# Kernel tuning notes

Hardware: AMD Instinct MI355X
Metric: run time of the kernel (lower is better)

## Reference

```python
import jax, jax.numpy as jnp
import numpy as np

N = 100000      # nodes
E = 800000      # edges
IN1 = 128       # gcn input feature dim
IN2 = 64        # lstm input feature dim
H = 128         # hidden_channels
B = 32          # lstm batch
T = 200         # lstm seq len
OUT = 1         # out_channels
TARGET = jnp.array([0, 1000, 2000, 3000, 4000, 5000, 6000, 7000])  # numgcnE=8


def setup_inputs() -> dict:
    key = jax.random.key(0)
    ks = jax.random.split(key, 20)
    s = 0.05
    inp = {
        "data0": jax.random.normal(ks[0], (B, T, IN2), jnp.float32),
        "data1": jax.random.normal(ks[1], (N, IN1), jnp.float32),
        "edge_index": jax.random.randint(ks[2], (2, E), 0, N, dtype=jnp.int64),
        # GCNConv layers (weight stored [in, out])
        "W1": jax.random.normal(ks[3], (IN1, H), jnp.float32) * s,
        "b1": jnp.zeros((H,), jnp.float32),
        "W2": jax.random.normal(ks[4], (H, H), jnp.float32) * s,
        "b2": jnp.zeros((H,), jnp.float32),
        # LSTM1 (gate order i,f,g,o as in torch)
        "Wih1": jax.random.normal(ks[5], (4 * H, IN2), jnp.float32) * s,
        "Whh1": jax.random.normal(ks[6], (4 * H, H), jnp.float32) * s,
        "bih1": jnp.zeros((4 * H,), jnp.float32),
        "bhh1": jnp.zeros((4 * H,), jnp.float32),
        # LSTM2
        "Wih2": jax.random.normal(ks[7], (4 * H, H), jnp.float32) * s,
        "Whh2": jax.random.normal(ks[8], (4 * H, H), jnp.float32) * s,
        "bih2": jnp.zeros((4 * H,), jnp.float32),
        "bhh2": jnp.zeros((4 * H,), jnp.float32),
        # MLP head: (numgcnE+1)*H -> (numgcnE+1)*H/2 -> OUT
        "m1_w": jax.random.normal(ks[9], (9 * H, 9 * H // 2), jnp.float32) * s,
        "m1_b": jnp.zeros((9 * H // 2,), jnp.float32),
        "m2_w": jax.random.normal(ks[10], (9 * H // 2, OUT), jnp.float32) * s,
        "m2_b": jnp.zeros((OUT,), jnp.float32),
    }
    return inp


def gcn_conv(x, W, b, src, dst, n):
    # PyG GCNConv: self-loops + symmetric normalization, then scatter-add.
    xw = x @ W                                                     # [N, H]
    ones = jnp.ones(src.shape[0], xw.dtype)
    deg = jax.ops.segment_sum(ones, dst, num_segments=n) + 1.0     # +1 self-loop
    dinv = jax.lax.rsqrt(deg)                                      # [N]
    norm = dinv[src] * dinv[dst]                                   # [E]
    agg = jax.ops.segment_sum(xw[src] * norm[:, None], dst, num_segments=n)
    agg = agg + xw * (dinv * dinv)[:, None]                        # self-loop msgs
    return agg + b


def lstm_final(x_tbi, Wih, Whh, bih, bhh):
    # x_tbi: [T, Bsz, in]; returns final hidden state h_T [Bsz, H]
    Bsz = x_tbi.shape[1]
    Hh = Whh.shape[1]
    bias = bih + bhh

    def step(carry, xt):
        h, c = carry
        g = xt @ Wih.T + h @ Whh.T + bias                          # [Bsz, 4H]
        i, f, gg, o = jnp.split(g, 4, axis=-1)
        c = jax.nn.sigmoid(f) * c + jax.nn.sigmoid(i) * jnp.tanh(gg)
        h = jax.nn.sigmoid(o) * jnp.tanh(c)
        return (h, c), None

    init = (jnp.zeros((Bsz, Hh), x_tbi.dtype), jnp.zeros((Bsz, Hh), x_tbi.dtype))
    (h, c), _ = jax.lax.scan(step, init, x_tbi)
    return h


def reference(data0, data1, edge_index, W1, b1, W2, b2,
              Wih1, Whh1, bih1, bhh1, Wih2, Whh2, bih2, bhh2,
              m1_w, m1_b, m2_w, m2_b):
    src, dst = edge_index[0], edge_index[1]
    n = data1.shape[0]
    # two GCN layers with ReLU
    h = jax.nn.relu(gcn_conv(data1, W1, b1, src, dst, n))
    h = jax.nn.relu(gcn_conv(h, W2, b2, src, dst, n))
    g = h[TARGET].reshape(-1)                                      # [numgcnE*H]
    # lstm1 over [B, T, IN2] (batch_first) -> final h_n [B, H]
    h1 = lstm_final(jnp.swapaxes(data0, 0, 1), Wih1, Whh1, bih1, bhh1)
    # lstm2 consumes h_n[None] as [batch=1, seq=B, H] -> final h [1, H]
    h2 = lstm_final(h1[:, None, :], Wih2, Whh2, bih2, bhh2)[0]     # [H]
    d = jnp.concatenate([g, h2])                                   # [(numgcnE+1)*H]
    return (d @ m1_w + m1_b) @ m2_w + m2_b                         # [OUT]
```

## Files before the change

### kernel.cpp

```cpp
#include <hip/hip_runtime.h>
#include <hip/hip_bf16.h>
#include <cstring>

using bf16 = __hip_bfloat16;
typedef _Float16 h2v __attribute__((ext_vector_type(2)));
typedef _Float16 h8v __attribute__((ext_vector_type(8)));

#if __has_builtin(__builtin_amdgcn_fdot2)
__device__ __forceinline__ float FDOT2(h2v a, h2v b, float c) {
    return __builtin_amdgcn_fdot2(a, b, c, false);
}
#else
__device__ __forceinline__ float FDOT2(h2v a, h2v b, float c) {
    return c + (float)a.x * (float)b.x + (float)a.y * (float)b.y;
}
#endif

__device__ __forceinline__ float sigm_f(float x) {
    return __builtin_amdgcn_rcpf(1.f + __expf(-x));
}
__device__ __forceinline__ float tanh_f(float x) {
    return 1.f - 2.f * __builtin_amdgcn_rcpf(1.f + __expf(2.f * x));
}

constexpr int NH    = 128;
constexpr int G4    = 512;
constexpr int TSEQ  = 200;
constexpr int BBATCH= 32;
constexpr int NTGT  = 8;

constexpr int LCAP1 = 1024;
constexpr int S1CAP = LCAP1 + NTGT;
constexpr int LCAP2 = 8192;
constexpr int S2CAP = LCAP2 + S1CAP;

constexpr size_t algn(size_t x) { return (x + 255) & ~size_t(255); }
constexpr size_t OFF_GX1  = 0;
constexpr size_t OFF_GX2  = algn(OFF_GX1  + 6400ull * G4 * 4);
constexpr size_t OFF_DEG  = algn(OFF_GX2  + 32ull * G4 * 4);
constexpr size_t OFF_DINV = algn(OFF_DEG  + 100000ull * 4);
constexpr size_t OFF_SL1  = algn(OFF_DINV + 100000ull * 4);
constexpr size_t OFF_SL2  = algn(OFF_SL1  + 100000ull * 4);
constexpr size_t OFF_CNT  = algn(OFF_SL2  + 100000ull * 4);
constexpr size_t OFF_L1   = algn(OFF_CNT  + 64);
constexpr size_t OFF_S1   = algn(OFF_L1   + (size_t)LCAP1 * 8);
constexpr size_t OFF_L2   = algn(OFF_S1   + (size_t)S1CAP * 4);
constexpr size_t OFF_S2   = algn(OFF_L2   + (size_t)LCAP2 * 8);
constexpr size_t OFF_XW1  = algn(OFF_S2   + (size_t)S2CAP * 4);
constexpr size_t OFF_H1   = algn(OFF_XW1  + (size_t)S2CAP * NH * 4);
constexpr size_t OFF_XW2  = algn(OFF_H1   + (size_t)S1CAP * NH * 4);
constexpr size_t OFF_DVEC = algn(OFF_XW2  + (size_t)S1CAP * NH * 4);
constexpr size_t OFF_H1F  = algn(OFF_DVEC + 1152ull * 4);
constexpr size_t OFF_CACC = algn(OFF_H1F  + 32ull * NH * 4);
constexpr size_t WS_NEEDED = OFF_CACC + 576ull * 4;

__device__ __forceinline__ int edge_at(const int* ei, int E, int is64, int row, int e) {
    return is64 ? ei[(((size_t)row * E) + e) * 2] : ei[((size_t)row * E) + e];
}

__device__ __forceinline__ float dinv_of(const int* deg, int v) {
    return rsqrtf((float)deg[v] + 1.0f);
}

__global__ void k_canary(unsigned int* out, unsigned int bits) {
    if (threadIdx.x == 0) out[0] = bits;
}


__global__ void k_init(const int* ei, int* deg, int* slot1, int* slot2, int* cnt,
                       float* colacc, int n) {
    int i = blockIdx.x * 256 + threadIdx.x;
    if (i < 14) cnt[i] = 0;
    if (i == 15) cnt[15] = (ei[1] == 0 && ei[3] == 0 && ei[5] == 0 && ei[7] == 0) ? 1 : 0;
    if (i < 576) colacc[i] = 0.f;
    for (; i < n; i += gridDim.x * 256) { deg[i] = 0; slot1[i] = -1; slot2[i] = -1; }
}

__global__ void k_deg_l1(const int* ei, int E, int* deg, int2* l1, int* cnt) {
    int is64 = cnt[15];
    for (int e = blockIdx.x * 256 + threadIdx.x; e < E; e += gridDim.x * 256) {
        int d = edge_at(ei, E, is64, 1, e);
        if ((unsigned)d < 100000u) atomicAdd(&deg[d], 1);
        if (d <= 7000 && d >= 0 && d % 1000 == 0) {
            int s = edge_at(ei, E, is64, 0, e);
            int idx = atomicAdd(&cnt[0], 1);
            if (idx < LCAP1) l1[idx] = make_int2(s, d);
        }
    }
}

__global__ void k_s1(const int2* l1, int* cnt, int* slot1, int* s1list,
                     int* slot2, int* s2list) {
    __shared__ int ns1;
    if (threadIdx.x == 0) ns1 = 0;
    __syncthreads();
    int m = min(cnt[0], LCAP1);
    for (int i = threadIdx.x; i < NTGT + m; i += blockDim.x) {
        int v = (i < NTGT) ? i * 1000 : l1[i - NTGT].x;
        if ((unsigned)v >= 100000u) continue;
        int old = atomicCAS(&slot1[v], -1, -2);
        if (old == -1) {
            int idx = atomicAdd(&ns1, 1);
            if (idx < S1CAP) { s1list[idx] = v; atomicExch(&slot1[v], idx); }
        }
    }
    __syncthreads();
    int n1 = min(ns1, S1CAP);
    if (threadIdx.x == 0) cnt[1] = n1;
    for (int i = threadIdx.x; i < n1; i += blockDim.x) {
        int v = s1list[i];
        int old = atomicCAS(&slot2[v], -1, -2);
        if (old == -1) {
            int idx = atomicAdd(&cnt[2], 1);
            if (idx < S2CAP) { s2list[idx] = v; atomicExch(&slot2[v], idx); }
        }
    }
}

__global__ void k_l2(const int* ei, int E, const int* slot1,
                     int2* l2, int* cnt, int* slot2, int* s2list) {
    int is64 = cnt[15];
    for (int e = blockIdx.x * 256 + threadIdx.x; e < E; e += gridDim.x * 256) {
        int d = edge_at(ei, E, is64, 1, e);
        if ((unsigned)d >= 100000u) continue;
        if (slot1[d] >= 0) {
            int s = edge_at(ei, E, is64, 0, e);
            if ((unsigned)s >= 100000u) continue;
            int idx = atomicAdd(&cnt[3], 1);
            if (idx < LCAP2) l2[idx] = make_int2(s, d);
            int old = atomicCAS(&slot2[s], -1, -2);
            if (old == -1) {
                int j = atomicAdd(&cnt[2], 1);
                if (j < S2CAP) { s2list[j] = s; atomicExch(&slot2[s], j); }
            }
        }
    }
}


__global__ void k_xw1(const float* x, const float* W, const int* s2list, const int* cnt, float* xw1) {
    int i = blockIdx.x;
    if (i >= min(cnt[2], S2CAP)) return;
    int node = s2list[i];
    __shared__ float xs[NH];
    int c = threadIdx.x;
    xs[c] = x[(size_t)node * NH + c];
    __syncthreads();
    float acc = 0.f;
    #pragma unroll 8
    for (int k = 0; k < NH; k++) acc += xs[k] * W[(size_t)k * NH + c];
    xw1[(size_t)i * NH + c] = acc;
}

__global__ void k_h1init(const float* xw1, const int* s1list, const int* cnt,
                         const int* slot2, const int* deg, float* h1) {
    int i = blockIdx.x;
    if (i >= min(cnt[1], S1CAP)) return;
    int node = s1list[i];
    int s2 = slot2[node];
    if (s2 < 0 || s2 >= S2CAP) s2 = 0;
    float v = dinv_of(deg, node);
    h1[i * NH + threadIdx.x] = xw1[(size_t)s2 * NH + threadIdx.x] * v * v;
}

__global__ void k_h1scat(const float* xw1, const int2* l2, const int* cnt,
                         const int* slot1, const int* slot2, const int* deg, float* h1) {
    int e = blockIdx.x;
    if (e >= min(cnt[3], LCAP2)) return;
    int2 sd = l2[e];
    int t1 = slot1[sd.y], s2 = slot2[sd.x];
    if (t1 < 0 || t1 >= S1CAP || s2 < 0 || s2 >= S2CAP) return;
    float w = dinv_of(deg, sd.x) * dinv_of(deg, sd.y);
    atomicAdd(&h1[t1 * NH + threadIdx.x],
              xw1[(size_t)s2 * NH + threadIdx.x] * w);
}

__global__ void k_xw2(const float* h1, const float* W, const float* b1, const int* cnt, float* xw2) {
    int i = blockIdx.x;
    if (i >= min(cnt[1], S1CAP)) return;
    __shared__ float xs[NH];
    int c = threadIdx.x;
    xs[c] = fmaxf(h1[i * NH + c] + b1[c], 0.f);
    __syncthreads();
    float acc = 0.f;
    #pragma unroll 8
    for (int k = 0; k < NH; k++) acc += xs[k] * W[(size_t)k * NH + c];
    xw2[(size_t)i * NH + c] = acc;
}

__global__ void k_gout(const float* xw2, const int2* l1, const int* cnt,
                       const int* slot1, const int* deg, const float* b2, float* dvec) {
    int t = blockIdx.x;
    int tgt = t * 1000;
    int c = threadIdx.x;
    float vt = dinv_of(deg, tgt);
    int st = slot1[tgt]; if (st < 0 || st >= S1CAP) st = 0;
    float acc = xw2[(size_t)st * NH + c] * vt * vt;
    int m = min(cnt[0], LCAP1);
    for (int e = 0; e < m; e++) {
        int2 sd = l1[e];
        if (sd.y == tgt) {
            int ss = slot1[sd.x];
            if (ss >= 0 && ss < S1CAP)
                acc += xw2[(size_t)ss * NH + c] * dinv_of(deg, sd.x) * vt;
        }
    }
    acc += b2[c];
    dvec[t * NH + c] = fmaxf(acc, 0.f);
}


__global__ __launch_bounds__(256) void k_gx1(const float* data0, const float* Wih,
                                             const float* bih, const float* bhh, float* gx) {
    constexpr int LDP = 68;
    __shared__ float As[64 * LDP];
    __shared__ float Bs[64 * LDP];
    int tid = threadIdx.x;
    int rb = blockIdx.x >> 3;
    int gb = blockIdx.x & 7;
    int r0 = rb * 64, g0 = gb * 64;
    for (int i = tid; i < 64 * 64; i += 256) {
        int rr = i >> 6, k = i & 63;
        int r = r0 + rr, b = r & 31, t = r >> 5;
        As[rr * LDP + k] = data0[((size_t)b * TSEQ + t) * 64 + k];
        Bs[rr * LDP + k] = Wih[(size_t)(g0 + rr) * 64 + k];
    }
    __syncthreads();
    int tr = (tid & 15) * 4;
    int tg = (tid >> 4) * 4;
    float acc[4][4] = {};
    #pragma unroll
    for (int k4 = 0; k4 < 16; k4++) {
        float4 a0 = *(const float4*)&As[(tr + 0) * LDP + k4 * 4];
        float4 a1 = *(const float4*)&As[(tr + 1) * LDP + k4 * 4];
        float4 a2 = *(const float4*)&As[(tr + 2) * LDP + k4 * 4];
        float4 a3 = *(const float4*)&As[(tr + 3) * LDP + k4 * 4];
        float4 b0 = *(const float4*)&Bs[(tg + 0) * LDP + k4 * 4];
        float4 b1 = *(const float4*)&Bs[(tg + 1) * LDP + k4 * 4];
        float4 b2 = *(const float4*)&Bs[(tg + 2) * LDP + k4 * 4];
        float4 b3 = *(const float4*)&Bs[(tg + 3) * LDP + k4 * 4];
        const float4 av[4] = {a0, a1, a2, a3};
        const float4 bv[4] = {b0, b1, b2, b3};
        #pragma unroll
        for (int i = 0; i < 4; i++)
            #pragma unroll
            for (int j = 0; j < 4; j++)
                acc[i][j] += av[i].x * bv[j].x + av[i].y * bv[j].y
                           + av[i].z * bv[j].z + av[i].w * bv[j].w;
    }
    float bias[4];
    #pragma unroll
    for (int j = 0; j < 4; j++) bias[j] = bih[g0 + tg + j] + bhh[g0 + tg + j];
    #pragma unroll
    for (int i = 0; i < 4; i++) {
        size_t row = (size_t)(r0 + tr + i) * G4 + g0 + tg;
        #pragma unroll
        for (int j = 0; j < 4; j++) gx[row + j] = acc[i][j] + bias[j];
    }
}

__global__ void k_gx2(const float* h1f, const float* Wih,
                      const float* bih, const float* bhh, float* gx) {
    int t = blockIdx.x;
    __shared__ float xs[NH];
    int tid = threadIdx.x;
    int g0 = tid, g1 = tid + 256;
    if (tid < NH) xs[tid] = h1f[t * NH + tid];
    __syncthreads();
    float a0 = bih[g0] + bhh[g0];
    float a1 = bih[g1] + bhh[g1];
    #pragma unroll 4
    for (int k = 0; k < NH; k++) {
        a0 += Wih[(size_t)g0 * NH + k] * xs[k];
        a1 += Wih[(size_t)g1 * NH + k] * xs[k];
    }
    gx[(size_t)t * G4 + g0] = a0;
    gx[(size_t)t * G4 + g1] = a1;
}

template<int T, int NB>
__global__ __launch_bounds__(256, 1) void k_lstm(const float* gx, const float* Whh, float* hfinal) {
    int b = blockIdx.x;
    int tid = threadIdx.x;
    int w = tid >> 6, l = tid & 63;
    int j = w * 32 + (l & 31);
    int role = l >> 5;
    int r0 = role ? (j + NH) : j;
    int r1 = role ? (j + 3 * NH) : (j + 2 * NH);
    __shared__ __align__(16) _Float16 hbuf[2][NH];
    h2v w0[NH / 2], w1[NH / 2];
    #pragma unroll
    for (int k = 0; k < NH; k += 4) {
        float4 a = *(const float4*)&Whh[(size_t)r0 * NH + k];
        w0[k / 2]     = h2v{(_Float16)a.x, (_Float16)a.y};
        w0[k / 2 + 1] = h2v{(_Float16)a.z, (_Float16)a.w};
        float4 c4 = *(const float4*)&Whh[(size_t)r1 * NH + k];
        w1[k / 2]     = h2v{(_Float16)c4.x, (_Float16)c4.y};
        w1[k / 2 + 1] = h2v{(_Float16)c4.z, (_Float16)c4.w};
    }
    if (tid < NH) { hbuf[0][tid] = (_Float16)0.f; hbuf[1][tid] = (_Float16)0.f; }
    float c = 0.f, hout = 0.f;
    float nx0 = gx[((size_t)0 * NB + b) * G4 + r0];
    float nx1 = gx[((size_t)0 * NB + b) * G4 + r1];
    __syncthreads();
    for (int t = 0; t < T; t++) {
        const h8v* hv8 = (const h8v*)hbuf[t & 1];
        float a0 = nx0, a1 = nx1;
        int tn = (t + 1 < T) ? (t + 1) : t;
        nx0 = gx[((size_t)tn * NB + b) * G4 + r0];
        nx1 = gx[((size_t)tn * NB + b) * G4 + r1];
        float p0 = 0.f, q0 = 0.f, p1 = 0.f, q1 = 0.f;
        #pragma unroll
        for (int m = 0; m < NH / 8; m++) {
            h8v h8 = hv8[m];
            h2v ha = __builtin_shufflevector(h8, h8, 0, 1);
            h2v hb = __builtin_shufflevector(h8, h8, 2, 3);
            h2v hc = __builtin_shufflevector(h8, h8, 4, 5);
            h2v hd = __builtin_shufflevector(h8, h8, 6, 7);
            p0 = FDOT2(w0[4 * m],     ha, p0);
            q0 = FDOT2(w0[4 * m + 1], hb, q0);
            p0 = FDOT2(w0[4 * m + 2], hc, p0);
            q0 = FDOT2(w0[4 * m + 3], hd, q0);
            p1 = FDOT2(w1[4 * m],     ha, p1);
            q1 = FDOT2(w1[4 * m + 1], hb, q1);
            p1 = FDOT2(w1[4 * m + 2], hc, p1);
            q1 = FDOT2(w1[4 * m + 3], hd, q1);
        }
        float ga = a0 + p0 + q0;
        float gb = a1 + p1 + q1;
        float s  = sigm_f(ga);
        float tg = role ? sigm_f(gb) : tanh_f(gb);
        float u  = s * tg;
        float fv = __shfl_xor(s,  32);
        float ov = __shfl_xor(tg, 32);
        if (role == 0) {
            c = fv * c + u;
            hout = ov * tanh_f(c);
            hbuf[(t + 1) & 1][j] = (_Float16)hout;
        }
        __syncthreads();
    }
    if (role == 0) hfinal[(size_t)b * NH + j] = hout;
}

__global__ __launch_bounds__(64) void k_head1(const float* dvec, const float* m1w, float* colacc) {
    int rg = blockIdx.x & 7;
    int cg = blockIdx.x >> 3;
    int col = cg * 64 + threadIdx.x;
    int r0 = rg * 144;
    float acc = 0.f;
    #pragma unroll 4
    for (int i = r0; i < r0 + 144; i++)
        acc += dvec[i] * m1w[(size_t)i * 576 + col];
    atomicAdd(&colacc[col], acc);
}

__global__ __launch_bounds__(256) void k_head2(const float* colacc, const float* m1b,
                                               const float* m2w, const float* m2b,
                                               unsigned int* out) {
    __shared__ float wr[4];
    int j = threadIdx.x;
    float sum = 0.f;
    for (int col = j; col < 576; col += 256)
        sum += (colacc[col] + m1b[col]) * m2w[col];
    #pragma unroll
    for (int off = 32; off > 0; off >>= 1) sum += __shfl_down(sum, off, 64);
    if ((j & 63) == 0) wr[j >> 6] = sum;
    __syncthreads();
    if (j == 0) {
        float s = wr[0] + wr[1] + wr[2] + wr[3] + m2b[0];
        bf16 hb = __float2bfloat16(s);
        unsigned short u;
        memcpy(&u, &hb, 2);
        out[0] = ((unsigned int)u << 16) | u;
    }
}


extern "C" void kernel_launch(void* const* d_in, const int* in_sizes, int n_in,
                              void* d_out, int out_size, void* d_ws, size_t ws_size,
                              hipStream_t stream) {
    const float* data0 = (const float*)d_in[0];
    const float* data1 = (const float*)d_in[1];
    const int*   ei    = (const int*)d_in[2];
    const float* W1    = (const float*)d_in[3];
    const float* b1    = (const float*)d_in[4];
    const float* W2    = (const float*)d_in[5];
    const float* b2    = (const float*)d_in[6];
    const float* Wih1  = (const float*)d_in[7];
    const float* Whh1  = (const float*)d_in[8];
    const float* bih1  = (const float*)d_in[9];
    const float* bhh1  = (const float*)d_in[10];
    const float* Wih2  = (const float*)d_in[11];
    const float* Whh2  = (const float*)d_in[12];
    const float* bih2  = (const float*)d_in[13];
    const float* bhh2  = (const float*)d_in[14];
    const float* m1w   = (const float*)d_in[15];
    const float* m1b   = (const float*)d_in[16];
    const float* m2w   = (const float*)d_in[17];
    const float* m2b   = (const float*)d_in[18];

    const int n = in_sizes[1] / NH;
    const int E = in_sizes[2] / 2;

    char* ws = (char*)d_ws;
    float* gx1   = (float*)(ws + OFF_GX1);
    float* gx2   = (float*)(ws + OFF_GX2);
    int*   deg   = (int*)  (ws + OFF_DEG);
    int*   slot1 = (int*)  (ws + OFF_SL1);
    int*   slot2 = (int*)  (ws + OFF_SL2);
    int*   cnt   = (int*)  (ws + OFF_CNT);
    int2*  l1    = (int2*) (ws + OFF_L1);
    int*   s1l   = (int*)  (ws + OFF_S1);
    int2*  l2    = (int2*) (ws + OFF_L2);
    int*   s2l   = (int*)  (ws + OFF_S2);
    float* xw1   = (float*)(ws + OFF_XW1);
    float* h1    = (float*)(ws + OFF_H1);
    float* xw2   = (float*)(ws + OFF_XW2);
    float* dvec  = (float*)(ws + OFF_DVEC);
    float* h1f   = (float*)(ws + OFF_H1F);
    float* cacc  = (float*)(ws + OFF_CACC);

    float v = 1.0f + (ws_size < WS_NEEDED ? 1.0f : 0.0f) + (n_in != 19 ? 2.0f : 0.0f);
    unsigned int fb; memcpy(&fb, &v, 4);
    unsigned int hi = fb >> 16;
    unsigned int canary_bits = (hi << 16) | hi;
    k_canary <<<1, 64, 0, stream>>>((unsigned int*)d_out, canary_bits);

    int nb = (n + 255) / 256;
    int eb = (E + 255) / 256;

    k_init   <<<nb, 256, 0, stream>>>(ei, deg, slot1, slot2, cnt, cacc, n);
    k_deg_l1 <<<eb, 256, 0, stream>>>(ei, E, deg, l1, cnt);
    k_s1     <<<1, 256, 0, stream>>>(l1, cnt, slot1, s1l, slot2, s2l);
    k_l2     <<<eb, 256, 0, stream>>>(ei, E, slot1, l2, cnt, slot2, s2l);
    k_xw1    <<<S2CAP, NH, 0, stream>>>(data1, W1, s2l, cnt, xw1);
    k_h1init <<<S1CAP, NH, 0, stream>>>(xw1, s1l, cnt, slot2, deg, h1);
    k_h1scat <<<LCAP2, NH, 0, stream>>>(xw1, l2, cnt, slot1, slot2, deg, h1);
    k_xw2    <<<S1CAP, NH, 0, stream>>>(h1, W2, b1, cnt, xw2);
    k_gout   <<<NTGT, NH, 0, stream>>>(xw2, l1, cnt, slot1, deg, b2, dvec);
    k_gx1    <<<800, 256, 0, stream>>>(data0, Wih1, bih1, bhh1, gx1);
    k_lstm<TSEQ, BBATCH><<<BBATCH, 256, 0, stream>>>(gx1, Whh1, h1f);
    k_gx2    <<<BBATCH, 256, 0, stream>>>(h1f, Wih2, bih2, bhh2, gx2);
    k_lstm<BBATCH, 1>  <<<1, 256, 0, stream>>>(gx2, Whh2, dvec + 1024);
    k_head1  <<<72, 64, 0, stream>>>(dvec, m1w, cacc);
    k_head2  <<<1, 256, 0, stream>>>(cacc, m1b, m2w, m2b, (unsigned int*)d_out);
    (void)out_size;
}
```

Measured before the change: 403.3 us.

## Fuse GCN pipeline into one cooperative kernel with grid syncs

Result: slower. 802.5 us (+99.0%).

```diff
diff --git a/kernel.cpp b/kernel.cpp
--- a/kernel.cpp
+++ b/kernel.cpp
@@ -1,6 +1,9 @@
 #include <hip/hip_runtime.h>
+#include <hip/hip_cooperative_groups.h>
 #include <hip/hip_bf16.h>
 #include <cstring>
+
+namespace cg = cooperative_groups;
 
 using bf16 = __hip_bfloat16;
 typedef _Float16 h2v __attribute__((ext_vector_type(2)));
@@ -21,6 +24,18 @@
 }
 __device__ __forceinline__ float tanh_f(float x) {
     return 1.f - 2.f * __builtin_amdgcn_rcpf(1.f + __expf(2.f * x));
+}
+
+__device__ __forceinline__ float xor32_get(float x) {
+#if __has_builtin(__builtin_amdgcn_permlane32_swap)
+    typedef unsigned uv2 __attribute__((ext_vector_type(2)));
+    union { float f; unsigned u; } cv; cv.f = x;
+    uv2 r = __builtin_amdgcn_permlane32_swap(cv.u, cv.u, false, false);
+    union { unsigned u; float f; } rv; rv.u = r[1];
+    return rv.f;
+#else
+    return __shfl_xor(x, 32);
+#endif
 }
 
 constexpr int NH    = 128;
@@ -33,6 +48,8 @@
 constexpr int S1CAP = LCAP1 + NTGT;
 constexpr int LCAP2 = 8192;
 constexpr int S2CAP = LCAP2 + S1CAP;
+
+constexpr int GCN_BLOCKS = 512;
 
 constexpr size_t algn(size_t x) { return (x + 255) & ~size_t(255); }
 constexpr size_t OFF_GX1  = 0;
@@ -62,151 +79,155 @@
     return rsqrtf((float)deg[v] + 1.0f);
 }
 
-__global__ void k_canary(unsigned int* out, unsigned int bits) {
-    if (threadIdx.x == 0) out[0] = bits;
-}
-
-
-__global__ void k_init(const int* ei, int* deg, int* slot1, int* slot2, int* cnt,
-                       float* colacc, int n) {
-    int i = blockIdx.x * 256 + threadIdx.x;
-    if (i < 14) cnt[i] = 0;
-    if (i == 15) cnt[15] = (ei[1] == 0 && ei[3] == 0 && ei[5] == 0 && ei[7] == 0) ? 1 : 0;
-    if (i < 576) colacc[i] = 0.f;
-    for (; i < n; i += gridDim.x * 256) { deg[i] = 0; slot1[i] = -1; slot2[i] = -1; }
-}
-
-__global__ void k_deg_l1(const int* ei, int E, int* deg, int2* l1, int* cnt) {
-    int is64 = cnt[15];
-    for (int e = blockIdx.x * 256 + threadIdx.x; e < E; e += gridDim.x * 256) {
-        int d = edge_at(ei, E, is64, 1, e);
-        if ((unsigned)d < 100000u) atomicAdd(&deg[d], 1);
+
+struct GcnArgs {
+    const int* ei; int E; int n;
+    int* deg; int* slot1; int* slot2; int* cnt;
+    int2* l1; int* s1l; int2* l2; int* s2l;
+    const float* data1; const float* W1; const float* b1;
+    const float* W2; const float* b2;
+    float* xw1; float* h1; float* xw2; float* dvec; float* colacc;
+    unsigned int* out; unsigned int canary;
+};
+
+__global__ __launch_bounds__(256) void k_gcn(GcnArgs a) {
+    cg::grid_group grid = cg::this_grid();
+    const int tid = threadIdx.x;
+    const int gid = blockIdx.x * 256 + tid;
+    const int gstride = gridDim.x * 256;
+    const int half = tid >> 7;
+    const int c    = tid & 127;
+
+    if (gid == 0) a.out[0] = a.canary;
+    if (gid < 14) a.cnt[gid] = 0;
+    if (gid == 15) a.cnt[15] = (a.ei[1] == 0 && a.ei[3] == 0 && a.ei[5] == 0 && a.ei[7] == 0) ? 1 : 0;
+    if (gid < 576) a.colacc[gid] = 0.f;
+    for (int i = gid; i < a.n; i += gstride) { a.deg[i] = 0; a.slot1[i] = -1; a.slot2[i] = -1; }
+    for (int i = gid; i < S1CAP * NH; i += gstride) a.h1[i] = 0.f;
+    grid.sync();
+
+    const int is64 = a.cnt[15];
+    for (int e = gid; e < a.E; e += gstride) {
+        int d = edge_at(a.ei, a.E, is64, 1, e);
+        if ((unsigned)d < 100000u) atomicAdd(&a.deg[d], 1);
         if (d <= 7000 && d >= 0 && d % 1000 == 0) {
-            int s = edge_at(ei, E, is64, 0, e);
-            int idx = atomicAdd(&cnt[0], 1);
-            if (idx < LCAP1) l1[idx] = make_int2(s, d);
-        }
-    }
-}
-
-__global__ void k_s1(const int2* l1, int* cnt, int* slot1, int* s1list,
-                     int* slot2, int* s2list) {
+            int s = edge_at(a.ei, a.E, is64, 0, e);
+            int idx = atomicAdd(&a.cnt[0], 1);
+            if (idx < LCAP1) a.l1[idx] = make_int2(s, d);
+        }
+    }
+    grid.sync();
+
     __shared__ int ns1;
-    if (threadIdx.x == 0) ns1 = 0;
-    __syncthreads();
-    int m = min(cnt[0], LCAP1);
-    for (int i = threadIdx.x; i < NTGT + m; i += blockDim.x) {
-        int v = (i < NTGT) ? i * 1000 : l1[i - NTGT].x;
-        if ((unsigned)v >= 100000u) continue;
-        int old = atomicCAS(&slot1[v], -1, -2);
-        if (old == -1) {
-            int idx = atomicAdd(&ns1, 1);
-            if (idx < S1CAP) { s1list[idx] = v; atomicExch(&slot1[v], idx); }
-        }
-    }
-    __syncthreads();
-    int n1 = min(ns1, S1CAP);
-    if (threadIdx.x == 0) cnt[1] = n1;
-    for (int i = threadIdx.x; i < n1; i += blockDim.x) {
-        int v = s1list[i];
-        int old = atomicCAS(&slot2[v], -1, -2);
-        if (old == -1) {
-            int idx = atomicAdd(&cnt[2], 1);
-            if (idx < S2CAP) { s2list[idx] = v; atomicExch(&slot2[v], idx); }
-        }
-    }
-}
-
-__global__ void k_l2(const int* ei, int E, const int* slot1,
-                     int2* l2, int* cnt, int* slot2, int* s2list) {
-    int is64 = cnt[15];
-    for (int e = blockIdx.x * 256 + threadIdx.x; e < E; e += gridDim.x * 256) {
-        int d = edge_at(ei, E, is64, 1, e);
+    if (blockIdx.x == 0) {
+        if (tid == 0) ns1 = 0;
+        __syncthreads();
+        int m = min(a.cnt[0], LCAP1);
+        for (int i = tid; i < NTGT + m; i += 256) {
+            int v = (i < NTGT) ? i * 1000 : a.l1[i - NTGT].x;
+            if ((unsigned)v >= 100000u) continue;
+            int old = atomicCAS(&a.slot1[v], -1, -2);
+            if (old == -1) {
+                int idx = atomicAdd(&ns1, 1);
+                if (idx < S1CAP) { a.s1l[idx] = v; atomicExch(&a.slot1[v], idx); }
+            }
+        }
+        __syncthreads();
+        int n1 = min(ns1, S1CAP);
+        if (tid == 0) a.cnt[1] = n1;
+        for (int i = tid; i < n1; i += 256) {
+            int v = a.s1l[i];
+            int old = atomicCAS(&a.slot2[v], -1, -2);
+            if (old == -1) {
+                int idx = atomicAdd(&a.cnt[2], 1);
+                if (idx < S2CAP) { a.s2l[idx] = v; atomicExch(&a.slot2[v], idx); }
+            }
+        }
+    }
+    grid.sync();
+
+    for (int e = gid; e < a.E; e += gstride) {
+        int d = edge_at(a.ei, a.E, is64, 1, e);
         if ((unsigned)d >= 100000u) continue;
-        if (slot1[d] >= 0) {
-            int s = edge_at(ei, E, is64, 0, e);
+        if (a.slot1[d] >= 0) {
+            int s = edge_at(a.ei, a.E, is64, 0, e);
             if ((unsigned)s >= 100000u) continue;
-            int idx = atomicAdd(&cnt[3], 1);
-            if (idx < LCAP2) l2[idx] = make_int2(s, d);
-            int old = atomicCAS(&slot2[s], -1, -2);
+            int idx = atomicAdd(&a.cnt[3], 1);
+            if (idx < LCAP2) a.l2[idx] = make_int2(s, d);
+            int old = atomicCAS(&a.slot2[s], -1, -2);
             if (old == -1) {
-                int j = atomicAdd(&cnt[2], 1);
-                if (j < S2CAP) { s2list[j] = s; atomicExch(&slot2[s], j); }
+                int j = atomicAdd(&a.cnt[2], 1);
+                if (j < S2CAP) { a.s2l[j] = s; atomicExch(&a.slot2[s], j); }
             }
         }
     }
-}
-
-
-__global__ void k_xw1(const float* x, const float* W, const int* s2list, const int* cnt, float* xw1) {
-    int i = blockIdx.x;
-    if (i >= min(cnt[2], S2CAP)) return;
-    int node = s2list[i];
-    __shared__ float xs[NH];
-    int c = threadIdx.x;
-    xs[c] = x[(size_t)node * NH + c];
-    __syncthreads();
-    float acc = 0.f;
-    #pragma unroll 8
-    for (int k = 0; k < NH; k++) acc += xs[k] * W[(size_t)k * NH + c];
-    xw1[(size_t)i * NH + c] = acc;
-}
-
-__global__ void k_h1init(const float* xw1, const int* s1list, const int* cnt,
-                         const int* slot2, const int* deg, float* h1) {
-    int i = blockIdx.x;
-    if (i >= min(cnt[1], S1CAP)) return;
-    int node = s1list[i];
-    int s2 = slot2[node];
-    if (s2 < 0 || s2 >= S2CAP) s2 = 0;
-    float v = dinv_of(deg, node);
-    h1[i * NH + threadIdx.x] = xw1[(size_t)s2 * NH + threadIdx.x] * v * v;
-}
-
-__global__ void k_h1scat(const float* xw1, const int2* l2, const int* cnt,
-                         const int* slot1, const int* slot2, const int* deg, float* h1) {
-    int e = blockIdx.x;
-    if (e >= min(cnt[3], LCAP2)) return;
-    int2 sd = l2[e];
-    int t1 = slot1[sd.y], s2 = slot2[sd.x];
-    if (t1 < 0 || t1 >= S1CAP || s2 < 0 || s2 >= S2CAP) return;
-    float w = dinv_of(deg, sd.x) * dinv_of(deg, sd.y);
-    atomicAdd(&h1[t1 * NH + threadIdx.x],
-              xw1[(size_t)s2 * NH + threadIdx.x] * w);
-}
-
-__global__ void k_xw2(const float* h1, const float* W, const float* b1, const int* cnt, float* xw2) {
-    int i = blockIdx.x;
-    if (i >= min(cnt[1], S1CAP)) return;
-    __shared__ float xs[NH];
-    int c = threadIdx.x;
-    xs[c] = fmaxf(h1[i * NH + c] + b1[c], 0.f);
-    __syncthreads();
-    float acc = 0.f;
-    #pragma unroll 8
-    for (int k = 0; k < NH; k++) acc += xs[k] * W[(size_t)k * NH + c];
-    xw2[(size_t)i * NH + c] = acc;
-}
-
-__global__ void k_gout(const float* xw2, const int2* l1, const int* cnt,
-                       const int* slot1, const int* deg, const float* b2, float* dvec) {
-    int t = blockIdx.x;
-    int tgt = t * 1000;
-    int c = threadIdx.x;
-    float vt = dinv_of(deg, tgt);
-    int st = slot1[tgt]; if (st < 0 || st >= S1CAP) st = 0;
-    float acc = xw2[(size_t)st * NH + c] * vt * vt;
-    int m = min(cnt[0], LCAP1);
-    for (int e = 0; e < m; e++) {
-        int2 sd = l1[e];
-        if (sd.y == tgt) {
-            int ss = slot1[sd.x];
-            if (ss >= 0 && ss < S1CAP)
-                acc += xw2[(size_t)ss * NH + c] * dinv_of(deg, sd.x) * vt;
-        }
-    }
-    acc += b2[c];
-    dvec[t * NH + c] = fmaxf(acc, 0.f);
+    grid.sync();
+
+    {
+        int m2 = min(a.cnt[2], S2CAP);
+        for (int i = blockIdx.x * 2 + half; i < m2; i += gridDim.x * 2) {
+            int node = a.s2l[i];
+            const float* xr = &a.data1[(size_t)node * NH];
+            float acc = 0.f;
+            #pragma unroll 8
+            for (int k = 0; k < NH; k++) acc += xr[k] * a.W1[(size_t)k * NH + c];
+            a.xw1[(size_t)i * NH + c] = acc;
+        }
+    }
+    grid.sync();
+
+    {
+        int m3 = min(a.cnt[3], LCAP2);
+        for (int e = blockIdx.x * 2 + half; e < m3; e += gridDim.x * 2) {
+            int2 sd = a.l2[e];
+            int t1 = a.slot1[sd.y], s2 = a.slot2[sd.x];
+            if (t1 < 0 || t1 >= S1CAP || s2 < 0 || s2 >= S2CAP) continue;
+            float wgt = dinv_of(a.deg, sd.x) * dinv_of(a.deg, sd.y);
+            atomicAdd(&a.h1[(size_t)t1 * NH + c], a.xw1[(size_t)s2 * NH + c] * wgt);
+        }
+    }
+    grid.sync();
+
+    {
+        int m1 = min(a.cnt[1], S1CAP);
+        for (int i = blockIdx.x * 2 + half; i < m1; i += gridDim.x * 2) {
+            int node = a.s1l[i];
+            int s2i = a.slot2[node];
+            if (s2i < 0 || s2i >= S2CAP) s2i = 0;
+            float v = dinv_of(a.deg, node);
+            float vv = v * v;
+            const float* hr = &a.h1[(size_t)i * NH];
+            const float* br = &a.xw1[(size_t)s2i * NH];
+            float acc = 0.f;
+            #pragma unroll 8
+            for (int k = 0; k < NH; k++) {
+                float xk = fmaxf(hr[k] + br[k] * vv + a.b1[k], 0.f);
+                acc += xk * a.W2[(size_t)k * NH + c];
+            }
+            a.xw2[(size_t)i * NH + c] = acc;
+        }
+    }
+    grid.sync();
+
+    {
+        int m = min(a.cnt[0], LCAP1);
+        for (int t = blockIdx.x * 2 + half; t < NTGT; t += gridDim.x * 2) {
+            int tgt = t * 1000;
+            float vt = dinv_of(a.deg, tgt);
+            int st = a.slot1[tgt]; if (st < 0 || st >= S1CAP) st = 0;
+            float acc = a.xw2[(size_t)st * NH + c] * vt * vt;
+            for (int e = 0; e < m; e++) {
+                int2 sd = a.l1[e];
+                if (sd.y == tgt) {
+                    int ss = a.slot1[sd.x];
+                    if (ss >= 0 && ss < S1CAP)
+                        acc += a.xw2[(size_t)ss * NH + c] * dinv_of(a.deg, sd.x) * vt;
+                }
+            }
+            acc += a.b2[c];
+            a.dvec[t * NH + c] = fmaxf(acc, 0.f);
+        }
+    }
 }
 
 
@@ -331,8 +352,8 @@
         float s  = sigm_f(ga);
         float tg = role ? sigm_f(gb) : tanh_f(gb);
         float u  = s * tg;
-        float fv = __shfl_xor(s,  32);
-        float ov = __shfl_xor(tg, 32);
+        float fv = xor32_get(s);
+        float ov = xor32_get(tg);
         if (role == 0) {
             c = fv * c + u;
             hout = ov * tanh_f(c);
@@ -425,20 +446,18 @@
     unsigned int fb; memcpy(&fb, &v, 4);
     unsigned int hi = fb >> 16;
     unsigned int canary_bits = (hi << 16) | hi;
-    k_canary <<<1, 64, 0, stream>>>((unsigned int*)d_out, canary_bits);
-
-    int nb = (n + 255) / 256;
-    int eb = (E + 255) / 256;
-
-    k_init   <<<nb, 256, 0, stream>>>(ei, deg, slot1, slot2, cnt, cacc, n);
-    k_deg_l1 <<<eb, 256, 0, stream>>>(ei, E, deg, l1, cnt);
-    k_s1     <<<1, 256, 0, stream>>>(l1, cnt, slot1, s1l, slot2, s2l);
-    k_l2     <<<eb, 256, 0, stream>>>(ei, E, slot1, l2, cnt, slot2, s2l);
-    k_xw1    <<<S2CAP, NH, 0, stream>>>(data1, W1, s2l, cnt, xw1);
-    k_h1init <<<S1CAP, NH, 0, stream>>>(xw1, s1l, cnt, slot2, deg, h1);
-    k_h1scat <<<LCAP2, NH, 0, stream>>>(xw1, l2, cnt, slot1, slot2, deg, h1);
-    k_xw2    <<<S1CAP, NH, 0, stream>>>(h1, W2, b1, cnt, xw2);
-    k_gout   <<<NTGT, NH, 0, stream>>>(xw2, l1, cnt, slot1, deg, b2, dvec);
+
+    GcnArgs ga;
+    ga.ei = ei; ga.E = E; ga.n = n;
+    ga.deg = deg; ga.slot1 = slot1; ga.slot2 = slot2; ga.cnt = cnt;
+    ga.l1 = l1; ga.s1l = s1l; ga.l2 = l2; ga.s2l = s2l;
+    ga.data1 = data1; ga.W1 = W1; ga.b1 = b1; ga.W2 = W2; ga.b2 = b2;
+    ga.xw1 = xw1; ga.h1 = h1; ga.xw2 = xw2; ga.dvec = dvec; ga.colacc = cacc;
+    ga.out = (unsigned int*)d_out; ga.canary = canary_bits;
+    void* gcn_params[1] = { &ga };
+    (void)hipLaunchCooperativeKernel((const void*)k_gcn, dim3(GCN_BLOCKS), dim3(256),
+                                     gcn_params, 0, stream);
+
     k_gx1    <<<800, 256, 0, stream>>>(data0, Wih1, bih1, bhh1, gx1);
     k_lstm<TSEQ, BBATCH><<<BBATCH, 256, 0, stream>>>(gx1, Whh1, h1f);
     k_gx2    <<<BBATCH, 256, 0, stream>>>(h1f, Wih2, bih2, bhh2, gx2);
```

## Fuse LSTM2 with head, precompute collapsed MLP weights, merge small kernels

Applied to the files above, without the earlier changes.

Result: slower. 480.4 us (+19.1%).

```diff
diff --git a/kernel.cpp b/kernel.cpp
--- a/kernel.cpp
+++ b/kernel.cpp
@@ -21,6 +21,18 @@
 }
 __device__ __forceinline__ float tanh_f(float x) {
     return 1.f - 2.f * __builtin_amdgcn_rcpf(1.f + __expf(2.f * x));
+}
+
+__device__ __forceinline__ float xor32_get(float x) {
+#if __has_builtin(__builtin_amdgcn_permlane32_swap)
+    typedef unsigned uv2 __attribute__((ext_vector_type(2)));
+    union { float f; unsigned u; } cv; cv.f = x;
+    uv2 r = __builtin_amdgcn_permlane32_swap(cv.u, cv.u, false, false);
+    union { unsigned u; float f; } rv; rv.u = r[1];
+    return rv.f;
+#else
+    return __shfl_xor(x, 32);
+#endif
 }
 
 constexpr int NH    = 128;
@@ -62,18 +74,15 @@
     return rsqrtf((float)deg[v] + 1.0f);
 }
 
-__global__ void k_canary(unsigned int* out, unsigned int bits) {
-    if (threadIdx.x == 0) out[0] = bits;
-}
-
-
 __global__ void k_init(const int* ei, int* deg, int* slot1, int* slot2, int* cnt,
-                       float* colacc, int n) {
-    int i = blockIdx.x * 256 + threadIdx.x;
-    if (i < 14) cnt[i] = 0;
-    if (i == 15) cnt[15] = (ei[1] == 0 && ei[3] == 0 && ei[5] == 0 && ei[7] == 0) ? 1 : 0;
-    if (i < 576) colacc[i] = 0.f;
-    for (; i < n; i += gridDim.x * 256) { deg[i] = 0; slot1[i] = -1; slot2[i] = -1; }
+                       float* h1, int n, unsigned int* out, unsigned int canary) {
+    int i0 = blockIdx.x * 256 + threadIdx.x;
+    int gstride = gridDim.x * 256;
+    if (i0 < 14) cnt[i0] = 0;
+    if (i0 == 15) cnt[15] = (ei[1] == 0 && ei[3] == 0 && ei[5] == 0 && ei[7] == 0) ? 1 : 0;
+    if (i0 == 16) out[0] = canary;
+    for (int i = i0; i < S1CAP * NH; i += gstride) h1[i] = 0.f;
+    for (int i = i0; i < n; i += gstride) { deg[i] = 0; slot1[i] = -1; slot2[i] = -1; }
 }
 
 __global__ void k_deg_l1(const int* ei, int E, int* deg, int2* l1, int* cnt) {
@@ -152,17 +161,6 @@
     xw1[(size_t)i * NH + c] = acc;
 }
 
-__global__ void k_h1init(const float* xw1, const int* s1list, const int* cnt,
-                         const int* slot2, const int* deg, float* h1) {
-    int i = blockIdx.x;
-    if (i >= min(cnt[1], S1CAP)) return;
-    int node = s1list[i];
-    int s2 = slot2[node];
-    if (s2 < 0 || s2 >= S2CAP) s2 = 0;
-    float v = dinv_of(deg, node);
-    h1[i * NH + threadIdx.x] = xw1[(size_t)s2 * NH + threadIdx.x] * v * v;
-}
-
 __global__ void k_h1scat(const float* xw1, const int2* l2, const int* cnt,
                          const int* slot1, const int* slot2, const int* deg, float* h1) {
     int e = blockIdx.x;
@@ -175,12 +173,18 @@
               xw1[(size_t)s2 * NH + threadIdx.x] * w);
 }
 
-__global__ void k_xw2(const float* h1, const float* W, const float* b1, const int* cnt, float* xw2) {
+__global__ void k_xw2(const float* h1, const float* xw1, const float* W, const float* b1,
+                      const int* cnt, const int* s1list, const int* slot2, const int* deg,
+                      float* xw2) {
     int i = blockIdx.x;
     if (i >= min(cnt[1], S1CAP)) return;
     __shared__ float xs[NH];
     int c = threadIdx.x;
-    xs[c] = fmaxf(h1[i * NH + c] + b1[c], 0.f);
+    int node = s1list[i];
+    int s2i = slot2[node];
+    if (s2i < 0 || s2i >= S2CAP) s2i = 0;
+    float v = dinv_of(deg, node);
+    xs[c] = fmaxf(h1[i * NH + c] + xw1[(size_t)s2i * NH + c] * (v * v) + b1[c], 0.f);
     __syncthreads();
     float acc = 0.f;
     #pragma unroll 8
@@ -210,12 +214,37 @@
 }
 
 
-__global__ __launch_bounds__(256) void k_gx1(const float* data0, const float* Wih,
-                                             const float* bih, const float* bhh, float* gx) {
+__global__ __launch_bounds__(256) void k_gx1hw(const float* data0, const float* Wih,
+                                               const float* bih, const float* bhh, float* gx,
+                                               const float* m1w, const float* m1b,
+                                               const float* m2w, const float* m2b, float* hw) {
+    int tid = threadIdx.x;
+    if (blockIdx.x >= 800) {
+        int hb = blockIdx.x - 800;
+        int wv = tid >> 6, ln = tid & 63;
+        if (hb < 18) {
+            #pragma unroll 4
+            for (int rr = 0; rr < 16; rr++) {
+                int row = hb * 64 + wv * 16 + rr;
+                float s = 0.f;
+                #pragma unroll
+                for (int j = ln; j < 576; j += 64) s += m1w[(size_t)row * 576 + j] * m2w[j];
+                #pragma unroll
+                for (int off = 32; off > 0; off >>= 1) s += __shfl_down(s, off, 64);
+                if (ln == 0) hw[row] = s;
+            }
+        } else if (wv == 0) {
+            float s = 0.f;
+            for (int j = ln; j < 576; j += 64) s += m1b[j] * m2w[j];
+            #pragma unroll
+            for (int off = 32; off > 0; off >>= 1) s += __shfl_down(s, off, 64);
+            if (ln == 0) hw[1152] = s + m2b[0];
+        }
+        return;
+    }
     constexpr int LDP = 68;
     __shared__ float As[64 * LDP];
     __shared__ float Bs[64 * LDP];
-    int tid = threadIdx.x;
     int rb = blockIdx.x >> 3;
     int gb = blockIdx.x & 7;
     int r0 = rb * 64, g0 = gb * 64;
@@ -257,25 +286,6 @@
         #pragma unroll
         for (int j = 0; j < 4; j++) gx[row + j] = acc[i][j] + bias[j];
     }
-}
-
-__global__ void k_gx2(const float* h1f, const float* Wih,
-                      const float* bih, const float* bhh, float* gx) {
-    int t = blockIdx.x;
-    __shared__ float xs[NH];
-    int tid = threadIdx.x;
-    int g0 = tid, g1 = tid + 256;
-    if (tid < NH) xs[tid] = h1f[t * NH + tid];
-    __syncthreads();
-    float a0 = bih[g0] + bhh[g0];
-    float a1 = bih[g1] + bhh[g1];
-    #pragma unroll 4
-    for (int k = 0; k < NH; k++) {
-        a0 += Wih[(size_t)g0 * NH + k] * xs[k];
-        a1 += Wih[(size_t)g1 * NH + k] * xs[k];
-    }
-    gx[(size_t)t * G4 + g0] = a0;
-    gx[(size_t)t * G4 + g1] = a1;
 }
 
 template<int T, int NB>
@@ -331,8 +341,8 @@
         float s  = sigm_f(ga);
         float tg = role ? sigm_f(gb) : tanh_f(gb);
         float u  = s * tg;
-        float fv = __shfl_xor(s,  32);
-        float ov = __shfl_xor(tg, 32);
+        float fv = xor32_get(s);
+        float ov = xor32_get(tg);
         if (role == 0) {
             c = fv * c + u;
             hout = ov * tanh_f(c);
@@ -343,33 +353,103 @@
     if (role == 0) hfinal[(size_t)b * NH + j] = hout;
 }
 
-__global__ __launch_bounds__(64) void k_head1(const float* dvec, const float* m1w, float* colacc) {
-    int rg = blockIdx.x & 7;
-    int cg = blockIdx.x >> 3;
-    int col = cg * 64 + threadIdx.x;
-    int r0 = rg * 144;
-    float acc = 0.f;
-    #pragma unroll 4
-    for (int i = r0; i < r0 + 144; i++)
-        acc += dvec[i] * m1w[(size_t)i * 576 + col];
-    atomicAdd(&colacc[col], acc);
-}
-
-__global__ __launch_bounds__(256) void k_head2(const float* colacc, const float* m1b,
-                                               const float* m2w, const float* m2b,
-                                               unsigned int* out) {
-    __shared__ float wr[4];
-    int j = threadIdx.x;
-    float sum = 0.f;
-    for (int col = j; col < 576; col += 256)
-        sum += (colacc[col] + m1b[col]) * m2w[col];
+__global__ __launch_bounds__(256, 1) void k_lstm2f(
+        const float* h1f, const float* Wih, const float* bih, const float* bhh,
+        const float* Whh, const float* dvec, const float* hw, unsigned int* out) {
+    __shared__ float hsf[32 * NH];
+    __shared__ float gxl[32 * G4];
+    __shared__ __align__(16) _Float16 hbuf[2][NH];
+    __shared__ float harr[NH];
+    __shared__ float red[4];
+    int tid = threadIdx.x;
+    for (int i = tid; i < 32 * NH; i += 256) hsf[i] = h1f[i];
+    if (tid < NH) { hbuf[0][tid] = (_Float16)0.f; hbuf[1][tid] = (_Float16)0.f; }
+    __syncthreads();
+    for (int gp = 0; gp < 2; gp++) {
+        int g = tid + gp * 256;
+        float wf[NH];
+        #pragma unroll
+        for (int k = 0; k < NH; k += 4) {
+            float4 a = *(const float4*)&Wih[(size_t)g * NH + k];
+            wf[k] = a.x; wf[k + 1] = a.y; wf[k + 2] = a.z; wf[k + 3] = a.w;
+        }
+        float bias = bih[g] + bhh[g];
+        for (int t = 0; t < 32; t++) {
+            const float4* hv4 = (const float4*)&hsf[t * NH];
+            float p = 0.f, q = 0.f;
+            #pragma unroll
+            for (int m = 0; m < NH / 4; m++) {
+                float4 h4 = hv4[m];
+                p += wf[4 * m] * h4.x + wf[4 * m + 1] * h4.y;
+                q += wf[4 * m + 2] * h4.z + wf[4 * m + 3] * h4.w;
+            }
+            gxl[t * G4 + g] = p + q + bias;
+        }
+    }
+    __syncthreads();
+    int w = tid >> 6, l = tid & 63;
+    int j = w * 32 + (l & 31);
+    int role = l >> 5;
+    int r0 = role ? (j + NH) : j;
+    int r1 = role ? (j + 3 * NH) : (j + 2 * NH);
+    h2v w0[NH / 2], w1[NH / 2];
     #pragma unroll
-    for (int off = 32; off > 0; off >>= 1) sum += __shfl_down(sum, off, 64);
-    if ((j & 63) == 0) wr[j >> 6] = sum;
-    __syncthreads();
-    if (j == 0) {
-        float s = wr[0] + wr[1] + wr[2] + wr[3] + m2b[0];
-        bf16 hb = __float2bfloat16(s);
+    for (int k = 0; k < NH; k += 4) {
+        float4 a = *(const float4*)&Whh[(size_t)r0 * NH + k];
+        w0[k / 2]     = h2v{(_Float16)a.x, (_Float16)a.y};
+        w0[k / 2 + 1] = h2v{(_Float16)a.z, (_Float16)a.w};
+        float4 c4 = *(const float4*)&Whh[(size_t)r1 * NH + k];
+        w1[k / 2]     = h2v{(_Float16)c4.x, (_Float16)c4.y};
+        w1[k / 2 + 1] = h2v{(_Float16)c4.z, (_Float16)c4.w};
+    }
+    float c = 0.f, hout = 0.f;
+    for (int t = 0; t < 32; t++) {
+        const h8v* hv8 = (const h8v*)hbuf[t & 1];
+        float a0 = gxl[t * G4 + r0];
+        float a1 = gxl[t * G4 + r1];
+        float p0 = 0.f, q0 = 0.f, p1 = 0.f, q1 = 0.f;
+        #pragma unroll
+        for (int m = 0; m < NH / 8; m++) {
+            h8v h8 = hv8[m];
+            h2v ha = __builtin_shufflevector(h8, h8, 0, 1);
+            h2v hb = __builtin_shufflevector(h8, h8, 2, 3);
+            h2v hc = __builtin_shufflevector(h8, h8, 4, 5);
+            h2v hd = __builtin_shufflevector(h8, h8, 6, 7);
+            p0 = FDOT2(w0[4 * m],     ha, p0);
+            q0 = FDOT2(w0[4 * m + 1], hb, q0);
+            p0 = FDOT2(w0[4 * m + 2], hc, p0);
+            q0 = FDOT2(w0[4 * m + 3], hd, q0);
+            p1 = FDOT2(w1[4 * m],     ha, p1);
+            q1 = FDOT2(w1[4 * m + 1], hb, q1);
+            p1 = FDOT2(w1[4 * m + 2], hc, p1);
+            q1 = FDOT2(w1[4 * m + 3], hd, q1);
+        }
+        float ga = a0 + p0 + q0;
+        float gb = a1 + p1 + q1;
+        float s  = sigm_f(ga);
+        float tg = role ? sigm_f(gb) : tanh_f(gb);
+        float u  = s * tg;
+        float fv = xor32_get(s);
+        float ov = xor32_get(tg);
+        if (role == 0) {
+            c = fv * c + u;
+            hout = ov * tanh_f(c);
+            hbuf[(t + 1) & 1][j] = (_Float16)hout;
+        }
+        __syncthreads();
+    }
+    if (role == 0) harr[j] = hout;
+    __syncthreads();
+    float s = 0.f;
+    for (int i = tid; i < 1024; i += 256) s += dvec[i] * hw[i];
+    if (tid < NH) s += harr[tid] * hw[1024 + tid];
+    #pragma unroll
+    for (int off = 32; off > 0; off >>= 1) s += __shfl_down(s, off, 64);
+    if ((tid & 63) == 0) red[tid >> 6] = s;
+    __syncthreads();
+    if (tid == 0) {
+        float tot = red[0] + red[1] + red[2] + red[3] + hw[1152];
+        bf16 hb = __float2bfloat16(tot);
         unsigned short u;
         memcpy(&u, &hb, 2);
         out[0] = ((unsigned int)u << 16) | u;
@@ -405,8 +485,8 @@
 
     char* ws = (char*)d_ws;
     float* gx1   = (float*)(ws + OFF_GX1);
-    float* gx2   = (float*)(ws + OFF_GX2);
     int*   deg   = (int*)  (ws + OFF_DEG);
+    float* hw    = (float*)(ws + OFF_DINV);
     int*   slot1 = (int*)  (ws + OFF_SL1);
     int*   slot2 = (int*)  (ws + OFF_SL2);
     int*   cnt   = (int*)  (ws + OFF_CNT);
@@ -419,31 +499,28 @@
     float* xw2   = (float*)(ws + OFF_XW2);
     float* dvec  = (float*)(ws + OFF_DVEC);
     float* h1f   = (float*)(ws + OFF_H1F);
-    float* cacc  = (float*)(ws + OFF_CACC);
 
     float v = 1.0f + (ws_size < WS_NEEDED ? 1.0f : 0.0f) + (n_in != 19 ? 2.0f : 0.0f);
     unsigned int fb; memcpy(&fb, &v, 4);
     unsigned int hi = fb >> 16;
     unsigned int canary_bits = (hi << 16) | hi;
-    k_canary <<<1, 64, 0, stream>>>((unsigned int*)d_out, canary_bits);
 
     int nb = (n + 255) / 256;
     int eb = (E + 255) / 256;
 
-    k_init   <<<nb, 256, 0, stream>>>(ei, deg, slot1, slot2, cnt, cacc, n);
+    k_init   <<<nb, 256, 0, stream>>>(ei, deg, slot1, slot2, cnt, h1, n,
+                                      (unsigned int*)d_out, canary_bits);
     k_deg_l1 <<<eb, 256, 0, stream>>>(ei, E, deg, l1, cnt);
     k_s1     <<<1, 256, 0, stream>>>(l1, cnt, slot1, s1l, slot2, s2l);
     k_l2     <<<eb, 256, 0, stream>>>(ei, E, slot1, l2, cnt, slot2, s2l);
     k_xw1    <<<S2CAP, NH, 0, stream>>>(data1, W1, s2l, cnt, xw1);
-    k_h1init <<<S1CAP, NH, 0, stream>>>(xw1, s1l, cnt, slot2, deg, h1);
     k_h1scat <<<LCAP2, NH, 0, stream>>>(xw1, l2, cnt, slot1, slot2, deg, h1);
-    k_xw2    <<<S1CAP, NH, 0, stream>>>(h1, W2, b1, cnt, xw2);
+    k_xw2    <<<S1CAP, NH, 0, stream>>>(h1, xw1, W2, b1, cnt, s1l, slot2, deg, xw2);
     k_gout   <<<NTGT, NH, 0, stream>>>(xw2, l1, cnt, slot1, deg, b2, dvec);
-    k_gx1    <<<800, 256, 0, stream>>>(data0, Wih1, bih1, bhh1, gx1);
+    k_gx1hw  <<<819, 256, 0, stream>>>(data0, Wih1, bih1, bhh1, gx1,
+                                       m1w, m1b, m2w, m2b, hw);
     k_lstm<TSEQ, BBATCH><<<BBATCH, 256, 0, stream>>>(gx1, Whh1, h1f);
-    k_gx2    <<<BBATCH, 256, 0, stream>>>(h1f, Wih2, bih2, bhh2, gx2);
-    k_lstm<BBATCH, 1>  <<<1, 256, 0, stream>>>(gx2, Whh2, dvec + 1024);
-    k_head1  <<<72, 64, 0, stream>>>(dvec, m1w, cacc);
-    k_head2  <<<1, 256, 0, stream>>>(cacc, m1b, m2w, m2b, (unsigned int*)d_out);
+    k_lstm2f <<<1, 256, 0, stream>>>(h1f, Wih2, bih2, bhh2, Whh2, dvec, hw,
+                                     (unsigned int*)d_out);
     (void)out_size;
 }
```
